# Performance work log

Hardware: AMD Instinct MI355X
Metric: run time of the kernel (lower is better)

The kernel has to match this reference:

```python
import jax, jax.numpy as jnp
import numpy as np

N = 300000   # total points
B = 8        # scenes per batch
INC = 64     # channels
HID = INC // 4  # MLP hidden (reduction=4)
S = 64       # voxel grid extent per axis


def _build_neighbor_table(batch_idx, coords):
    """Kernel map for a 3x3x3 stride-1 sparse conv: for each point, index of the
    point at each of the 27 integer offsets (N = missing -> zero pad row)."""
    base = S + 2
    keys = (((batch_idx.astype(np.int64) * base + coords[:, 0]) * base
             + coords[:, 1]) * base + coords[:, 2])
    order = np.argsort(keys)
    skeys = keys[order]
    offs = np.array([(dx, dy, dz) for dx in (-1, 0, 1)
                     for dy in (-1, 0, 1) for dz in (-1, 0, 1)], dtype=np.int64)
    off_keys = (offs[:, 0] * base + offs[:, 1]) * base + offs[:, 2]  # [27]
    q = keys[:, None] + off_keys[None, :]                             # [N,27]
    pos = np.searchsorted(skeys, q)
    posc = np.minimum(pos, N - 1)
    valid = (pos < N) & (skeys[posc] == q)
    nbr = np.where(valid, order[posc], N).astype(np.int32)
    return nbr


def setup_inputs() -> dict:
    rng = np.random.default_rng(0)
    batch_idx = np.sort(rng.integers(0, B, size=N)).astype(np.int32)
    coords = rng.integers(1, S - 1, size=(N, 3))
    nbr_idx = _build_neighbor_table(batch_idx, coords)
    key = jax.random.key(0)
    k = jax.random.split(key, 6)
    return {
        "F": jax.random.normal(k[0], (N, INC), dtype=jnp.float32),
        "batch_idx": jnp.asarray(batch_idx),
        "nbr_idx": jnp.asarray(nbr_idx),
        "W1": jax.random.normal(k[1], (INC, HID), dtype=jnp.float32) * 0.05,
        "b1": jax.random.normal(k[2], (HID,), dtype=jnp.float32) * 0.05,
        "W2": jax.random.normal(k[3], (HID, INC), dtype=jnp.float32) * 0.05,
        "b2": jax.random.normal(k[4], (INC,), dtype=jnp.float32) * 0.05,
        "conv_w": jax.random.normal(k[5], (27, 2, 1), dtype=jnp.float32) * 0.1,
    }


def reference(F, batch_idx, nbr_idx, W1, b1, W2, b2, conv_w):
    # ---- channel attention: per-batch segmented mean & max, broadcast back ----
    counts = jax.ops.segment_sum(jnp.ones((N,), F.dtype), batch_idx, num_segments=B)
    seg_mean = jax.ops.segment_sum(F, batch_idx, num_segments=B) / counts[:, None]
    seg_max = jax.ops.segment_max(F, batch_idx, num_segments=B)
    avg = seg_mean[batch_idx]   # [N, INC]
    mx = seg_max[batch_idx]     # [N, INC]

    def mlp(a):
        return jax.nn.relu(a @ W1 + b1) @ W2 + b2

    gate = jax.nn.sigmoid(mlp(avg) + mlp(mx))
    z = F * gate                # [N, INC]

    # ---- spatial attention: channel mean/max -> 2ch sparse 3^3 conv -> gate ----
    sm = jnp.stack([z.mean(axis=1), z.max(axis=1)], axis=1)   # [N, 2] (mean, max)
    smp = jnp.concatenate([sm, jnp.zeros((1, 2), sm.dtype)], axis=0)  # pad row N
    gathered = smp[nbr_idx]                                    # [N, 27, 2]
    c = jnp.einsum('nkc,kco->no', gathered, conv_w)            # [N, 1]
    return z * jax.nn.sigmoid(c)
```

## Files before the change

### kernel.cpp

```cpp
#include <hip/hip_runtime.h>
#include <math.h>

#define INC 64
#define HID 16
#define NB 8

__device__ __forceinline__ void atomicMaxF(float* addr, float val) {
    if (val >= 0.0f) atomicMax((int*)addr, __float_as_int(val));
    else             atomicMin((unsigned int*)addr, __float_as_uint(val));
}

__device__ __forceinline__ void acc4(float4& sum, float4& mx, const float4 v) {
    sum.x += v.x; sum.y += v.y; sum.z += v.z; sum.w += v.w;
    mx.x = fmaxf(mx.x, v.x); mx.y = fmaxf(mx.y, v.y);
    mx.z = fmaxf(mx.z, v.z); mx.w = fmaxf(mx.w, v.w);
}

__global__ void k_init(float* seg_sum, float* seg_max, int* counts, float* sm_pad) {
    int t = threadIdx.x;
    if (t < NB * INC) { seg_sum[t] = 0.0f; seg_max[t] = -INFINITY; }
    else if (t < NB * INC + NB) counts[t - NB * INC] = 0;
    else if (t < NB * INC + NB + 2) sm_pad[t - NB * INC - NB] = 0.0f;
}

__global__ void k_reduce(const float* __restrict__ F, const int* __restrict__ bidx,
                         float* __restrict__ seg_sum, float* __restrict__ seg_max,
                         int* __restrict__ counts, int N, int CHUNK) {
    __shared__ float4 lsum[4][16];
    __shared__ float4 lmax[4][16];

    int lane = threadIdx.x & 63;
    int wid  = threadIdx.x >> 6;
    int blockStart = blockIdx.x * (CHUNK * 4);
    if (blockStart >= N) return;
    int blockEnd = min(blockStart + CHUNK * 4, N);
    int start = blockStart + wid * CHUNK;
    bool active = start < N;
    int pend = active ? min(start + CHUNK, N) : start;

    int sub = lane >> 4;
    int ch  = (lane & 15) << 2;

    int bblk = bidx[blockStart];
    bool blockUniform = (bidx[blockEnd - 1] == bblk);

    if (blockUniform) {
        float4 s0 = make_float4(0.f,0.f,0.f,0.f), s1 = s0, s2 = s0, s3 = s0;
        float4 m0 = make_float4(-INFINITY,-INFINITY,-INFINITY,-INFINITY);
        float4 m1 = m0, m2 = m0, m3 = m0;
        if (active) {
            const float* fb = F + (size_t)sub * INC + ch;
            int p = start;
            #pragma unroll 1
            for (; p + 16 <= pend; p += 16) {
                const float* fp = fb + (size_t)p * INC;
                float4 v0 = *reinterpret_cast<const float4*>(fp);
                float4 v1 = *reinterpret_cast<const float4*>(fp + 4 * INC);
                float4 v2 = *reinterpret_cast<const float4*>(fp + 8 * INC);
                float4 v3 = *reinterpret_cast<const float4*>(fp + 12 * INC);
                __builtin_amdgcn_sched_barrier(0);
                acc4(s0, m0, v0); acc4(s1, m1, v1);
                acc4(s2, m2, v2); acc4(s3, m3, v3);
            }
            #pragma unroll 1
            for (; p < pend; p += 4) {
                float4 v = *reinterpret_cast<const float4*>(fb + (size_t)p * INC);
                acc4(s0, m0, v);
            }
        }
        s0.x += s1.x + s2.x + s3.x; s0.y += s1.y + s2.y + s3.y;
        s0.z += s1.z + s2.z + s3.z; s0.w += s1.w + s2.w + s3.w;
        m0.x = fmaxf(fmaxf(m0.x, m1.x), fmaxf(m2.x, m3.x));
        m0.y = fmaxf(fmaxf(m0.y, m1.y), fmaxf(m2.y, m3.y));
        m0.z = fmaxf(fmaxf(m0.z, m1.z), fmaxf(m2.z, m3.z));
        m0.w = fmaxf(fmaxf(m0.w, m1.w), fmaxf(m2.w, m3.w));
        #pragma unroll
        for (int msk = 16; msk < 64; msk <<= 1) {
            s0.x += __shfl_xor(s0.x, msk); s0.y += __shfl_xor(s0.y, msk);
            s0.z += __shfl_xor(s0.z, msk); s0.w += __shfl_xor(s0.w, msk);
            m0.x = fmaxf(m0.x, __shfl_xor(m0.x, msk));
            m0.y = fmaxf(m0.y, __shfl_xor(m0.y, msk));
            m0.z = fmaxf(m0.z, __shfl_xor(m0.z, msk));
            m0.w = fmaxf(m0.w, __shfl_xor(m0.w, msk));
        }
        if (lane < 16) { lsum[wid][lane] = s0; lmax[wid][lane] = m0; }
        __syncthreads();
        if (wid == 0 && lane < 16) {
            float4 a0 = lsum[0][lane], a1 = lsum[1][lane], a2 = lsum[2][lane], a3 = lsum[3][lane];
            float4 x0 = lmax[0][lane], x1 = lmax[1][lane], x2 = lmax[2][lane], x3 = lmax[3][lane];
            float4 S = make_float4(a0.x+a1.x+a2.x+a3.x, a0.y+a1.y+a2.y+a3.y,
                                   a0.z+a1.z+a2.z+a3.z, a0.w+a1.w+a2.w+a3.w);
            float4 M = make_float4(fmaxf(fmaxf(x0.x,x1.x),fmaxf(x2.x,x3.x)),
                                   fmaxf(fmaxf(x0.y,x1.y),fmaxf(x2.y,x3.y)),
                                   fmaxf(fmaxf(x0.z,x1.z),fmaxf(x2.z,x3.z)),
                                   fmaxf(fmaxf(x0.w,x1.w),fmaxf(x2.w,x3.w)));
            float* ss = seg_sum + bblk * INC + (lane << 2);
            atomicAdd(ss + 0, S.x); atomicAdd(ss + 1, S.y);
            atomicAdd(ss + 2, S.z); atomicAdd(ss + 3, S.w);
            float* sx = seg_max + bblk * INC + (lane << 2);
            atomicMaxF(sx + 0, M.x); atomicMaxF(sx + 1, M.y);
            atomicMaxF(sx + 2, M.z); atomicMaxF(sx + 3, M.w);
            if (lane == 0) atomicAdd(&counts[bblk], blockEnd - blockStart);
        }
        return;
    }

    if (!active) return;
    int bfirst = bidx[start];
    int blast  = bidx[pend - 1];

    if (bfirst == blast) {
        float4 sum = make_float4(0.f,0.f,0.f,0.f);
        float4 mx  = make_float4(-INFINITY,-INFINITY,-INFINITY,-INFINITY);
        const float* fb = F + (size_t)sub * INC + ch;
        #pragma unroll 1
        for (int p = start; p < pend; p += 4) {
            float4 v = *reinterpret_cast<const float4*>(fb + (size_t)p * INC);
            acc4(sum, mx, v);
        }
        #pragma unroll
        for (int msk = 16; msk < 64; msk <<= 1) {
            sum.x += __shfl_xor(sum.x, msk); sum.y += __shfl_xor(sum.y, msk);
            sum.z += __shfl_xor(sum.z, msk); sum.w += __shfl_xor(sum.w, msk);
            mx.x = fmaxf(mx.x, __shfl_xor(mx.x, msk));
            mx.y = fmaxf(mx.y, __shfl_xor(mx.y, msk));
            mx.z = fmaxf(mx.z, __shfl_xor(mx.z, msk));
            mx.w = fmaxf(mx.w, __shfl_xor(mx.w, msk));
        }
        if (sub == 0) {
            float* ss = seg_sum + bfirst * INC + ch;
            atomicAdd(ss + 0, sum.x); atomicAdd(ss + 1, sum.y);
            atomicAdd(ss + 2, sum.z); atomicAdd(ss + 3, sum.w);
            float* sx = seg_max + bfirst * INC + ch;
            atomicMaxF(sx + 0, mx.x); atomicMaxF(sx + 1, mx.y);
            atomicMaxF(sx + 2, mx.z); atomicMaxF(sx + 3, mx.w);
            if (lane == 0) atomicAdd(&counts[bfirst], pend - start);
        }
        return;
    }

    bool isCnt = (lane & 15) == 0;
    float4 sum = make_float4(0.f,0.f,0.f,0.f);
    float4 mx  = make_float4(-INFINITY,-INFINITY,-INFINITY,-INFINITY);
    int cnt = 0, cur = -1;
    for (int p = start; p < pend; p += 4) {
        int pp = p + sub;
        int b = bidx[pp];
        if (b != cur) {
            if (cur >= 0) {
                float* ss = seg_sum + cur * INC + ch;
                atomicAdd(ss + 0, sum.x); atomicAdd(ss + 1, sum.y);
                atomicAdd(ss + 2, sum.z); atomicAdd(ss + 3, sum.w);
                float* sx = seg_max + cur * INC + ch;
                atomicMaxF(sx + 0, mx.x); atomicMaxF(sx + 1, mx.y);
                atomicMaxF(sx + 2, mx.z); atomicMaxF(sx + 3, mx.w);
                if (isCnt && cnt) atomicAdd(&counts[cur], cnt);
            }
            sum = make_float4(0.f,0.f,0.f,0.f);
            mx  = make_float4(-INFINITY,-INFINITY,-INFINITY,-INFINITY);
            cnt = 0; cur = b;
        }
        const float4 v = *reinterpret_cast<const float4*>(F + (size_t)pp * INC + ch);
        acc4(sum, mx, v);
        cnt += (int)isCnt;
    }
    if (cur >= 0) {
        float* ss = seg_sum + cur * INC + ch;
        atomicAdd(ss + 0, sum.x); atomicAdd(ss + 1, sum.y);
        atomicAdd(ss + 2, sum.z); atomicAdd(ss + 3, sum.w);
        float* sx = seg_max + cur * INC + ch;
        atomicMaxF(sx + 0, mx.x); atomicMaxF(sx + 1, mx.y);
        atomicMaxF(sx + 2, mx.z); atomicMaxF(sx + 3, mx.w);
        if (isCnt && cnt) atomicAdd(&counts[cur], cnt);
    }
}

__global__ void k_gate(const float* __restrict__ seg_sum, const float* __restrict__ seg_max,
                       const int* __restrict__ counts,
                       const float* __restrict__ W1, const float* __restrict__ b1,
                       const float* __restrict__ W2, const float* __restrict__ b2,
                       float* __restrict__ gate) {
    __shared__ float s_avg[NB * INC], s_mx[NB * INC];
    __shared__ float s_W1[INC * HID], s_W2[HID * INC];
    __shared__ float s_ha[NB * HID], s_hm[NB * HID];
    int t = threadIdx.x;
    s_W1[t] = W1[t]; s_W1[t + 512] = W1[t + 512];
    s_W2[t] = W2[t]; s_W2[t + 512] = W2[t + 512];
    {
        int b = t >> 6;
        float c = (float)counts[b];
        s_avg[t] = seg_sum[t] / c;
        s_mx[t]  = seg_max[t];
    }
    __syncthreads();
    if (t < NB * HID) {
        int b = t >> 4, j = t & (HID - 1);
        float ha = b1[j], hm = b1[j];
        #pragma unroll
        for (int c = 0; c < INC; ++c) {
            float w = s_W1[c * HID + j];
            ha += s_avg[b * INC + c] * w;
            hm += s_mx[b * INC + c] * w;
        }
        s_ha[t] = fmaxf(ha, 0.f);
        s_hm[t] = fmaxf(hm, 0.f);
    }
    __syncthreads();
    {
        int b = t >> 6, c = t & 63;
        float o = 2.f * b2[c];
        #pragma unroll
        for (int j = 0; j < HID; ++j)
            o += (s_ha[b * HID + j] + s_hm[b * HID + j]) * s_W2[j * INC + c];
        gate[t] = 1.f / (1.f + expf(-o));
    }
}

__global__ void k_sm(const float* __restrict__ F, const int* __restrict__ bidx,
                     const float* __restrict__ gate, float* __restrict__ sm,
                     int N, int CHUNK) {
    int lane = threadIdx.x & 63;
    int wave = (blockIdx.x * blockDim.x + threadIdx.x) >> 6;
    int start = wave * CHUNK;
    if (start >= N) return;
    int pend = min(start + CHUNK, N);
    int sub = lane >> 4, ch = (lane & 15) << 2;
    bool wr = (lane & 15) == 0;

    int bfirst = bidx[start];
    int blast  = bidx[pend - 1];

    if (bfirst == blast) {
        const float4 g = *reinterpret_cast<const float4*>(gate + bfirst * INC + ch);
        const float* fb = F + (size_t)sub * INC + ch;
        int p = start;
        #pragma unroll 1
        for (; p + 16 <= pend; p += 16) {
            const float* fp = fb + (size_t)p * INC;
            float4 v0 = *reinterpret_cast<const float4*>(fp);
            float4 v1 = *reinterpret_cast<const float4*>(fp + 4 * INC);
            float4 v2 = *reinterpret_cast<const float4*>(fp + 8 * INC);
            float4 v3 = *reinterpret_cast<const float4*>(fp + 12 * INC);
            __builtin_amdgcn_sched_barrier(0);
            float s0, s1, s2, s3, m0, m1, m2, m3;
            {
                float4 z = make_float4(v0.x*g.x, v0.y*g.y, v0.z*g.z, v0.w*g.w);
                s0 = z.x + z.y + z.z + z.w; m0 = fmaxf(fmaxf(z.x, z.y), fmaxf(z.z, z.w));
            }
            {
                float4 z = make_float4(v1.x*g.x, v1.y*g.y, v1.z*g.z, v1.w*g.w);
                s1 = z.x + z.y + z.z + z.w; m1 = fmaxf(fmaxf(z.x, z.y), fmaxf(z.z, z.w));
            }
            {
                float4 z = make_float4(v2.x*g.x, v2.y*g.y, v2.z*g.z, v2.w*g.w);
                s2 = z.x + z.y + z.z + z.w; m2 = fmaxf(fmaxf(z.x, z.y), fmaxf(z.z, z.w));
            }
            {
                float4 z = make_float4(v3.x*g.x, v3.y*g.y, v3.z*g.z, v3.w*g.w);
                s3 = z.x + z.y + z.z + z.w; m3 = fmaxf(fmaxf(z.x, z.y), fmaxf(z.z, z.w));
            }
            #pragma unroll
            for (int msk = 1; msk < 16; msk <<= 1) {
                s0 += __shfl_xor(s0, msk); m0 = fmaxf(m0, __shfl_xor(m0, msk));
                s1 += __shfl_xor(s1, msk); m1 = fmaxf(m1, __shfl_xor(m1, msk));
                s2 += __shfl_xor(s2, msk); m2 = fmaxf(m2, __shfl_xor(m2, msk));
                s3 += __shfl_xor(s3, msk); m3 = fmaxf(m3, __shfl_xor(m3, msk));
            }
            if (wr) {
                *reinterpret_cast<float2*>(sm + (size_t)(p + sub) * 2)      = make_float2(s0 * (1.f/64.f), m0);
                *reinterpret_cast<float2*>(sm + (size_t)(p + 4 + sub) * 2)  = make_float2(s1 * (1.f/64.f), m1);
                *reinterpret_cast<float2*>(sm + (size_t)(p + 8 + sub) * 2)  = make_float2(s2 * (1.f/64.f), m2);
                *reinterpret_cast<float2*>(sm + (size_t)(p + 12 + sub) * 2) = make_float2(s3 * (1.f/64.f), m3);
            }
        }
        #pragma unroll 1
        for (; p < pend; p += 4) {
            float4 v = *reinterpret_cast<const float4*>(fb + (size_t)p * INC);
            float4 z = make_float4(v.x*g.x, v.y*g.y, v.z*g.z, v.w*g.w);
            float s = z.x + z.y + z.z + z.w;
            float m = fmaxf(fmaxf(z.x, z.y), fmaxf(z.z, z.w));
            #pragma unroll
            for (int msk = 1; msk < 16; msk <<= 1) {
                s += __shfl_xor(s, msk); m = fmaxf(m, __shfl_xor(m, msk));
            }
            if (wr) *reinterpret_cast<float2*>(sm + (size_t)(p + sub) * 2) = make_float2(s * (1.f/64.f), m);
        }
        return;
    }

    for (int p = start; p < pend; p += 4) {
        int pp = p + sub;
        int b = bidx[pp];
        float4 v = *reinterpret_cast<const float4*>(F + (size_t)pp * INC + ch);
        float4 g = *reinterpret_cast<const float4*>(gate + b * INC + ch);
        float4 z = make_float4(v.x*g.x, v.y*g.y, v.z*g.z, v.w*g.w);
        float s = z.x + z.y + z.z + z.w;
        float m = fmaxf(fmaxf(z.x, z.y), fmaxf(z.z, z.w));
        #pragma unroll
        for (int msk = 1; msk < 16; msk <<= 1) {
            s += __shfl_xor(s, msk); m = fmaxf(m, __shfl_xor(m, msk));
        }
        if (wr) *reinterpret_cast<float2*>(sm + (size_t)pp * 2) = make_float2(s * (1.f/64.f), m);
    }
}

__global__ void k_out(const float* __restrict__ F, const int* __restrict__ bidx,
                      const int* __restrict__ nbr, const float* __restrict__ gate,
                      const float* __restrict__ sm, const float* __restrict__ cw,
                      float* __restrict__ out, int N, int CHUNK) {
    int lane = threadIdx.x & 63;
    int j = lane & 15;
    int sub = lane >> 4, ch = (lane & 15) << 2;
    float2 cwa = make_float2(cw[2 * j], cw[2 * j + 1]);
    float2 cwb = (j < 11) ? make_float2(cw[2 * (16 + j)], cw[2 * (16 + j) + 1])
                          : make_float2(0.f, 0.f);
    int wave = (blockIdx.x * blockDim.x + threadIdx.x) >> 6;
    int start = wave * CHUNK;
    if (start >= N) return;
    int pend = min(start + CHUNK, N);

    int bfirst = bidx[start];
    int blast  = bidx[pend - 1];

    if (bfirst == blast) {
        const float4 g = *reinterpret_cast<const float4*>(gate + bfirst * INC + ch);
        int pp = start + sub;
        int i1 = nbr[pp * 27 + j];
        int i2 = (j < 11) ? nbr[pp * 27 + 16 + j] : N;
        #pragma unroll 1
        for (int p = start; p < pend; p += 4) {
            float2 a = *reinterpret_cast<const float2*>(sm + (size_t)i1 * 2);
            float2 b = *reinterpret_cast<const float2*>(sm + (size_t)i2 * 2);
            int np = p + 4 + sub; if (np >= N) np = N - 1;
            int ni1 = nbr[np * 27 + j];
            int ni2 = (j < 11) ? nbr[np * 27 + 16 + j] : N;
            float4 v = *reinterpret_cast<const float4*>(F + (size_t)(p + sub) * INC + ch);
            __builtin_amdgcn_sched_barrier(0);
            float cpart = a.x * cwa.x + a.y * cwa.y + b.x * cwb.x + b.y * cwb.y;
            #pragma unroll
            for (int msk = 1; msk < 16; msk <<= 1) cpart += __shfl_xor(cpart, msk);
            float sig = 1.f / (1.f + expf(-cpart));
            float4 o = make_float4(v.x * g.x * sig, v.y * g.y * sig,
                                   v.z * g.z * sig, v.w * g.w * sig);
            *reinterpret_cast<float4*>(out + (size_t)(p + sub) * INC + ch) = o;
            i1 = ni1; i2 = ni2;
        }
        return;
    }

    for (int p = start; p < pend; p += 4) {
        int pp = p + sub;
        int rb = pp * 27;
        int i1 = nbr[rb + j];
        int i2 = (j < 11) ? nbr[rb + 16 + j] : N;
        float2 a = *reinterpret_cast<const float2*>(sm + (size_t)i1 * 2);
        float2 b = *reinterpret_cast<const float2*>(sm + (size_t)i2 * 2);
        float cpart = a.x * cwa.x + a.y * cwa.y + b.x * cwb.x + b.y * cwb.y;
        #pragma unroll
        for (int msk = 1; msk < 16; msk <<= 1) cpart += __shfl_xor(cpart, msk);
        float sig = 1.f / (1.f + expf(-cpart));
        int bb = bidx[pp];
        float4 v = *reinterpret_cast<const float4*>(F + (size_t)pp * INC + ch);
        float4 g = *reinterpret_cast<const float4*>(gate + bb * INC + ch);
        float4 o = make_float4(v.x * g.x * sig, v.y * g.y * sig,
                               v.z * g.z * sig, v.w * g.w * sig);
        *reinterpret_cast<float4*>(out + (size_t)pp * INC + ch) = o;
    }
}

extern "C" void kernel_launch(void* const* d_in, const int* in_sizes, int n_in,
                              void* d_out, int out_size, void* d_ws, size_t ws_size,
                              hipStream_t stream) {
    const float* F    = (const float*)d_in[0];
    const int*   bidx = (const int*)d_in[1];
    const int*   nbr  = (const int*)d_in[2];
    const float* W1   = (const float*)d_in[3];
    const float* b1   = (const float*)d_in[4];
    const float* W2   = (const float*)d_in[5];
    const float* b2   = (const float*)d_in[6];
    const float* cw   = (const float*)d_in[7];
    float* out = (float*)d_out;
    int N = in_sizes[1];

    float* ws      = (float*)d_ws;
    float* seg_sum = ws;
    float* seg_max = ws + NB * INC;
    int*   counts  = (int*)(ws + 2 * NB * INC);
    float* gate    = ws + 2 * NB * INC + 16;
    float* sm      = ws + 3 * NB * INC + 32;

    k_init<<<1, 1024, 0, stream>>>(seg_sum, seg_max, counts, sm + (size_t)N * 2);

    {
        const int waves = 2048;
        int chunk = ((N + waves * 16 - 1) / (waves * 16)) * 16;
        int blocks = (N + chunk * 4 - 1) / (chunk * 4);
        k_reduce<<<blocks, 256, 0, stream>>>(F, bidx, seg_sum, seg_max, counts, N, chunk);
    }

    k_gate<<<1, 512, 0, stream>>>(seg_sum, seg_max, counts, W1, b1, W2, b2, gate);

    {
        const int waves = 4096;
        int chunk = ((N + waves * 16 - 1) / (waves * 16)) * 16;
        int blocks = (N + chunk * 4 - 1) / (chunk * 4);
        k_sm<<<blocks, 256, 0, stream>>>(F, bidx, gate, sm, N, chunk);
        k_out<<<blocks, 256, 0, stream>>>(F, bidx, nbr, gate, sm, cw, out, N, chunk);
    }
}
```

Baseline: 250.9 us.

## Widen reduce blocks to 16 waves and deepen neighbor prefetch in output kernel

The reduction kernel now runs 1024-thread blocks of 16 waves with a fixed chunk of 48 rows per wave, combining 16 partials in shared memory so fewer blocks issue global atomics. The output kernel's uniform-batch path becomes a two-stage software pipeline. It prefetches the spatial mean/max values for the next rows and the neighbor indices two iterations ahead, hiding the dependent gather latency. Chunk sizes for the sm/out kernels are fixed at 32 rows per wave, which launches more waves, and the deeper prefetch adds register pressure.

```diff
diff --git a/kernel.cpp b/kernel.cpp
--- a/kernel.cpp
+++ b/kernel.cpp
@@ -23,17 +23,18 @@
     else if (t < NB * INC + NB + 2) sm_pad[t - NB * INC - NB] = 0.0f;
 }
 
-__global__ void k_reduce(const float* __restrict__ F, const int* __restrict__ bidx,
-                         float* __restrict__ seg_sum, float* __restrict__ seg_max,
-                         int* __restrict__ counts, int N, int CHUNK) {
-    __shared__ float4 lsum[4][16];
-    __shared__ float4 lmax[4][16];
+__global__ __launch_bounds__(1024)
+void k_reduce(const float* __restrict__ F, const int* __restrict__ bidx,
+              float* __restrict__ seg_sum, float* __restrict__ seg_max,
+              int* __restrict__ counts, int N, int CHUNK) {
+    __shared__ float4 lsum[16][16];
+    __shared__ float4 lmax[16][16];
 
     int lane = threadIdx.x & 63;
     int wid  = threadIdx.x >> 6;
-    int blockStart = blockIdx.x * (CHUNK * 4);
+    int blockStart = blockIdx.x * (CHUNK * 16);
     if (blockStart >= N) return;
-    int blockEnd = min(blockStart + CHUNK * 4, N);
+    int blockEnd = min(blockStart + CHUNK * 16, N);
     int start = blockStart + wid * CHUNK;
     bool active = start < N;
     int pend = active ? min(start + CHUNK, N) : start;
@@ -86,14 +87,15 @@
         if (lane < 16) { lsum[wid][lane] = s0; lmax[wid][lane] = m0; }
         __syncthreads();
         if (wid == 0 && lane < 16) {
-            float4 a0 = lsum[0][lane], a1 = lsum[1][lane], a2 = lsum[2][lane], a3 = lsum[3][lane];
-            float4 x0 = lmax[0][lane], x1 = lmax[1][lane], x2 = lmax[2][lane], x3 = lmax[3][lane];
-            float4 S = make_float4(a0.x+a1.x+a2.x+a3.x, a0.y+a1.y+a2.y+a3.y,
-                                   a0.z+a1.z+a2.z+a3.z, a0.w+a1.w+a2.w+a3.w);
-            float4 M = make_float4(fmaxf(fmaxf(x0.x,x1.x),fmaxf(x2.x,x3.x)),
-                                   fmaxf(fmaxf(x0.y,x1.y),fmaxf(x2.y,x3.y)),
-                                   fmaxf(fmaxf(x0.z,x1.z),fmaxf(x2.z,x3.z)),
-                                   fmaxf(fmaxf(x0.w,x1.w),fmaxf(x2.w,x3.w)));
+            float4 S = lsum[0][lane];
+            float4 M = lmax[0][lane];
+            #pragma unroll
+            for (int w = 1; w < 16; ++w) {
+                float4 a = lsum[w][lane], x = lmax[w][lane];
+                S.x += a.x; S.y += a.y; S.z += a.z; S.w += a.w;
+                M.x = fmaxf(M.x, x.x); M.y = fmaxf(M.y, x.y);
+                M.z = fmaxf(M.z, x.z); M.w = fmaxf(M.w, x.w);
+            }
             float* ss = seg_sum + bblk * INC + (lane << 2);
             atomicAdd(ss + 0, S.x); atomicAdd(ss + 1, S.y);
             atomicAdd(ss + 2, S.z); atomicAdd(ss + 3, S.w);
@@ -324,26 +326,31 @@
 
     if (bfirst == blast) {
         const float4 g = *reinterpret_cast<const float4*>(gate + bfirst * INC + ch);
-        int pp = start + sub;
-        int i1 = nbr[pp * 27 + j];
-        int i2 = (j < 11) ? nbr[pp * 27 + 16 + j] : N;
+        int pp0 = start + sub;
+        int i1 = nbr[pp0 * 27 + j];
+        int i2 = (j < 11) ? nbr[pp0 * 27 + 16 + j] : N;
+        float2 A  = *reinterpret_cast<const float2*>(sm + (size_t)i1 * 2);
+        float2 Bv = *reinterpret_cast<const float2*>(sm + (size_t)i2 * 2);
+        int np = pp0 + 4; if (np >= N) np = N - 1;
+        int n1 = nbr[np * 27 + j];
+        int n2 = (j < 11) ? nbr[np * 27 + 16 + j] : N;
         #pragma unroll 1
         for (int p = start; p < pend; p += 4) {
-            float2 a = *reinterpret_cast<const float2*>(sm + (size_t)i1 * 2);
-            float2 b = *reinterpret_cast<const float2*>(sm + (size_t)i2 * 2);
-            int np = p + 4 + sub; if (np >= N) np = N - 1;
-            int ni1 = nbr[np * 27 + j];
-            int ni2 = (j < 11) ? nbr[np * 27 + 16 + j] : N;
+            float2 A1 = *reinterpret_cast<const float2*>(sm + (size_t)n1 * 2);
+            float2 B1 = *reinterpret_cast<const float2*>(sm + (size_t)n2 * 2);
             float4 v = *reinterpret_cast<const float4*>(F + (size_t)(p + sub) * INC + ch);
+            int np2 = p + 8 + sub; if (np2 >= N) np2 = N - 1;
+            int nn1 = nbr[np2 * 27 + j];
+            int nn2 = (j < 11) ? nbr[np2 * 27 + 16 + j] : N;
             __builtin_amdgcn_sched_barrier(0);
-            float cpart = a.x * cwa.x + a.y * cwa.y + b.x * cwb.x + b.y * cwb.y;
+            float cpart = A.x * cwa.x + A.y * cwa.y + Bv.x * cwb.x + Bv.y * cwb.y;
             #pragma unroll
             for (int msk = 1; msk < 16; msk <<= 1) cpart += __shfl_xor(cpart, msk);
             float sig = 1.f / (1.f + expf(-cpart));
             float4 o = make_float4(v.x * g.x * sig, v.y * g.y * sig,
                                    v.z * g.z * sig, v.w * g.w * sig);
             *reinterpret_cast<float4*>(out + (size_t)(p + sub) * INC + ch) = o;
-            i1 = ni1; i2 = ni2;
+            A = A1; Bv = B1; n1 = nn1; n2 = nn2;
         }
         return;
     }
@@ -392,17 +399,15 @@
     k_init<<<1, 1024, 0, stream>>>(seg_sum, seg_max, counts, sm + (size_t)N * 2);
 
     {
-        const int waves = 2048;
-        int chunk = ((N + waves * 16 - 1) / (waves * 16)) * 16;
-        int blocks = (N + chunk * 4 - 1) / (chunk * 4);
-        k_reduce<<<blocks, 256, 0, stream>>>(F, bidx, seg_sum, seg_max, counts, N, chunk);
+        const int chunk = 48;
+        int blocks = (N + chunk * 16 - 1) / (chunk * 16);
+        k_reduce<<<blocks, 1024, 0, stream>>>(F, bidx, seg_sum, seg_max, counts, N, chunk);
     }
 
     k_gate<<<1, 512, 0, stream>>>(seg_sum, seg_max, counts, W1, b1, W2, b2, gate);
 
     {
-        const int waves = 4096;
-        int chunk = ((N + waves * 16 - 1) / (waves * 16)) * 16;
+        const int chunk = 32;
         int blocks = (N + chunk * 4 - 1) / (chunk * 4);
         k_sm<<<blocks, 256, 0, stream>>>(F, bidx, gate, sm, N, chunk);
         k_out<<<blocks, 256, 0, stream>>>(F, bidx, nbr, gate, sm, cw, out, N, chunk);
```

New measurement: 233.1 us. -7.1%, faster.
